# Kernel optimization log

Measured on AMD Instinct MI355X. Metric: run time of the kernel, lower is better.

The kernel has to match this reference:

```python
import jax, jax.numpy as jnp
import numpy as np

AXIAL_WEIGHT = 1.0
N_NODES = 1_000_000
N_ELEM = 2_000_000


def setup_inputs() -> dict:
    key = jax.random.key(0)
    ks = jax.random.split(key, 12)
    N, E = N_NODES, N_ELEM
    pred_raw = jax.random.normal(ks[0], (N, 3), jnp.float32)
    u_c = jax.random.uniform(ks[1], (1,), jnp.float32) + 0.5
    theta_c = jax.random.uniform(ks[2], (1,), jnp.float32) + 0.5
    connectivity = jax.random.randint(ks[3], (E, 2), 0, N, jnp.int32)
    # lengths / section properties bounded away from zero (1/L^3 appears)
    elem_lengths = jax.random.uniform(ks[4], (E,), jnp.float32) + 0.5
    prop_E = jax.random.uniform(ks[5], (E,), jnp.float32) + 1.0
    prop_A = jax.random.uniform(ks[6], (E,), jnp.float32) + 0.5
    prop_I22 = jax.random.uniform(ks[7], (E,), jnp.float32) + 0.5
    ang = jax.random.uniform(ks[8], (E,), jnp.float32) * (2.0 * np.pi)
    # columns: [cos, 0, sin] -- forward reads cols 0 and 2
    elem_directions = jnp.stack([jnp.cos(ang), jnp.zeros_like(ang), jnp.sin(ang)], axis=1)
    F_ext = jax.random.normal(ks[9], (N, 3), jnp.float32)
    bc_disp = (jax.random.uniform(ks[10], (N, 1)) < 0.05).astype(jnp.float32)
    bc_rot = (jax.random.uniform(ks[11], (N, 1)) < 0.05).astype(jnp.float32)
    return {
        "pred_raw": pred_raw, "u_c": u_c, "theta_c": theta_c,
        "elem_lengths": elem_lengths, "prop_E": prop_E, "prop_A": prop_A,
        "prop_I22": prop_I22, "elem_directions": elem_directions,
        "F_ext": F_ext, "bc_disp": bc_disp, "bc_rot": bc_rot,
        "connectivity": connectivity,
    }


def reference(pred_raw, u_c, theta_c, elem_lengths, prop_E, prop_A, prop_I22,
              elem_directions, F_ext, bc_disp, bc_rot, connectivity):
    n_nodes = pred_raw.shape[0]
    # physical displacements: [ux*u_c, uz*u_c, th*theta_c]
    scale = jnp.concatenate([u_c, u_c, theta_c])  # [3]
    u_phys = pred_raw * scale[None, :]

    nA = connectivity[:, 0]
    nB = connectivity[:, 1]
    c = elem_directions[:, 0]
    s = elem_directions[:, 2]
    L = elem_lengths
    EA = prop_E * prop_A
    EI = prop_E * prop_I22

    uA = u_phys[nA]  # [E,3] gather
    uB = u_phys[nB]
    u_A = c * uA[:, 0] + s * uA[:, 1]
    w_A = -s * uA[:, 0] + c * uA[:, 1]
    th_A = -uA[:, 2]
    u_B = c * uB[:, 0] + s * uB[:, 1]
    w_B = -s * uB[:, 0] + c * uB[:, 1]
    th_B = -uB[:, 2]

    ea_l = EA / L * AXIAL_WEIGHT
    ei_l = EI / L
    ei_l2 = EI / L**2
    ei_l3 = EI / L**3

    # analytic K_loc @ d_local (K_loc is the standard 6x6 beam stiffness)
    dw = w_A - w_B
    f0 = ea_l * (u_A - u_B)
    f1 = 12.0 * ei_l3 * dw + 6.0 * ei_l2 * (th_A + th_B)
    f2 = 6.0 * ei_l2 * dw + 4.0 * ei_l * th_A + 2.0 * ei_l * th_B
    f3 = -f0
    f4 = -f1
    f5 = 6.0 * ei_l2 * dw + 2.0 * ei_l * th_A + 4.0 * ei_l * th_B

    fA = jnp.stack([c * f0 - s * f1, s * f0 + c * f1, -f2], axis=1)  # [E,3]
    fB = jnp.stack([c * f3 - s * f4, s * f3 + c * f4, -f5], axis=1)

    F_int = jax.ops.segment_sum(
        jnp.concatenate([fA, fB], axis=0),
        jnp.concatenate([nA, nB], axis=0),
        num_segments=n_nodes)  # [N,3] scatter-add

    R = F_int - F_ext
    free_mask = jnp.concatenate([1.0 - bc_disp, 1.0 - bc_disp, 1.0 - bc_rot], axis=1)
    R_free = R * free_mask
    F_free = F_ext * free_mask
    F_norm_sq = jnp.maximum(jnp.sum(F_free**2), 1e-30)
    loss = jnp.sum(R_free**2) / F_norm_sq  # single graph -> n_graphs = 1
    return loss
```

## Files before the change

kernel.cpp:

```cpp
#include <hip/hip_runtime.h>
#include <hip/hip_fp16.h>


#define SPAN   1024
#define NBMAX  1024
#define OFFN   (NBMAX + 1)
#define FTH    1024
#define FBE    4096
#define REGR   8192
#define ATH    512

struct F3 { float x, y, z; };

__device__ __forceinline__ uint2 packrec(float fx, float fy, float fz, int local) {
    unsigned short hx = __half_as_ushort(__float2half(fx));
    unsigned short hy = __half_as_ushort(__float2half(fy));
    unsigned short hz = __half_as_ushort(__float2half(fz));
    return make_uint2(((unsigned)hy << 16) | hx, ((unsigned)local << 16) | hz);
}

__device__ __forceinline__ int block_incl_scan(int v, int* wsum, int lane, int wv) {
    #pragma unroll
    for (int off = 1; off < 64; off <<= 1) {
        int t = __shfl_up(v, off, 64);
        if (lane >= off) v += t;
    }
    if (lane == 63) wsum[wv] = v;
    __syncthreads();
    if (wv == 0) {
        int w = (lane < 16) ? wsum[lane] : 0;
        #pragma unroll
        for (int off = 1; off < 16; off <<= 1) {
            int t = __shfl_up(w, off, 64);
            if (lane >= off) w += t;
        }
        if (lane < 16) wsum[lane] = w;
    }
    __syncthreads();
    return v + ((wv > 0) ? wsum[wv - 1] : 0);
}

__global__ void __launch_bounds__(1024)
fill_kernel(const int2* __restrict__ conn,
            const F3*  __restrict__ pred,
            const float* __restrict__ u_c,
            const float* __restrict__ theta_c,
            const float* __restrict__ len,
            const float* __restrict__ pE,
            const float* __restrict__ pA,
            const float* __restrict__ pI,
            const float* __restrict__ dir,
            uint2* __restrict__ regions,
            unsigned short* __restrict__ offsTab,
            double* __restrict__ accSlots,
            int cs, int ce, int NB) {
    __shared__ uint2          slab[FBE];
    __shared__ unsigned short sbk [FBE];
    __shared__ int hist0[NBMAX];
    __shared__ int hist1[NBMAX];
    __shared__ int boff [NBMAX];
    __shared__ int sc   [NBMAX];
    __shared__ int wsum [16];

    int tid = threadIdx.x, lane = tid & 63, wv = tid >> 6;

    if (blockIdx.x == 0 && tid < 512) accSlots[tid] = 0.0;

    hist0[tid] = 0;
    hist1[tid] = 0;
    __syncthreads();

    float uc = u_c[0];
    float tc = theta_c[0];
    int bs = cs + blockIdx.x * FBE;
    int be = bs + FBE; if (be > ce) be = ce;

    unsigned sv[8];
    uint2    rc[8];

    #pragma unroll
    for (int j = 0; j < 4; ++j) {
        int e = bs + j * FTH + tid;
        unsigned sa = 0xFFFFFFFFu, sb = 0xFFFFFFFFu;
        if (e < be) {
            int2 cn = conn[e];
            int na = cn.x, nb = cn.y;

            F3 pa_ = pred[na];
            F3 pb_ = pred[nb];

            float c  = dir[3 * e + 0];
            float s  = dir[3 * e + 2];
            float L  = len[e];
            float Ee = pE[e];
            float EA = Ee * pA[e];
            float EI = Ee * pI[e];

            float a0 = pa_.x * uc;
            float a1 = pa_.y * uc;
            float a2 = pa_.z * tc;
            float b0 = pb_.x * uc;
            float b1 = pb_.y * uc;
            float b2 = pb_.z * tc;

            float u_A  =  c * a0 + s * a1;
            float w_A  = -s * a0 + c * a1;
            float th_A = -a2;
            float u_B  =  c * b0 + s * b1;
            float w_B  = -s * b0 + c * b1;
            float th_B = -b2;

            float invL  = 1.0f / L;
            float ea_l  = EA * invL;
            float ei_l  = EI * invL;
            float ei_l2 = ei_l  * invL;
            float ei_l3 = ei_l2 * invL;

            float dw = w_A - w_B;
            float f0 = ea_l * (u_A - u_B);
            float f1 = 12.0f * ei_l3 * dw + 6.0f * ei_l2 * (th_A + th_B);
            float f2 = 6.0f * ei_l2 * dw + 4.0f * ei_l * th_A + 2.0f * ei_l * th_B;
            float f5 = 6.0f * ei_l2 * dw + 2.0f * ei_l * th_A + 4.0f * ei_l * th_B;

            float fA0 = c * f0 - s * f1;
            float fA1 = s * f0 + c * f1;

            int* h = (j < 2) ? hist0 : hist1;

            int bkA = na >> 10;
            int rA  = atomicAdd(&h[bkA], 1);
            sa = ((unsigned)rA << 10) | (unsigned)bkA;
            rc[2 * j + 0] = packrec(fA0, fA1, -f2, na & 1023);

            int bkB = nb >> 10;
            int rB  = atomicAdd(&h[bkB], 1);
            sb = ((unsigned)rB << 10) | (unsigned)bkB;
            rc[2 * j + 1] = packrec(-fA0, -fA1, -f5, nb & 1023);
        }
        sv[2 * j + 0] = sa;
        sv[2 * j + 1] = sb;
    }
    __syncthreads();

    int h0 = hist0[tid], h1 = hist1[tid];
    int tot = h0 + h1;
    int iF = block_incl_scan(tot, wsum, lane, wv);
    boff[tid] = iF - tot;
    sc[tid]   = iF;
    __syncthreads();

    unsigned short* offs = offsTab + (size_t)blockIdx.x * OFFN;
    if (tid < NB) offs[tid] = (unsigned short)boff[tid];
    if (tid == 0) offs[NB]  = (unsigned short)sc[NB - 1];

    uint2* regbase = regions + (size_t)blockIdx.x * REGR;

    int i0 = block_incl_scan(h0, wsum, lane, wv);
    sc[tid] = i0;
    __syncthreads();
    #pragma unroll
    for (int r = 0; r < 4; ++r) {
        unsigned s2 = sv[r];
        if (s2 != 0xFFFFFFFFu) {
            int bk = (int)(s2 & 1023u);
            int rk = (int)(s2 >> 10);
            int slot = sc[bk] - hist0[bk] + rk;
            slab[slot] = rc[r];
            sbk[slot]  = (unsigned short)bk;
        }
    }
    __syncthreads();
    int tot0 = sc[NBMAX - 1];
    for (int i = tid; i < tot0; i += FTH) {
        int bk = sbk[i];
        regbase[boff[bk] + (i - (sc[bk] - hist0[bk]))] = slab[i];
    }
    __syncthreads();

    int i1 = block_incl_scan(h1, wsum, lane, wv);
    sc[tid] = i1;
    __syncthreads();
    #pragma unroll
    for (int r = 4; r < 8; ++r) {
        unsigned s2 = sv[r];
        if (s2 != 0xFFFFFFFFu) {
            int bk = (int)(s2 & 1023u);
            int rk = (int)(s2 >> 10);
            int slot = sc[bk] - hist1[bk] + rk;
            slab[slot] = rc[r];
            sbk[slot]  = (unsigned short)bk;
        }
    }
    __syncthreads();
    int tot1 = sc[NBMAX - 1];
    for (int i = tid; i < tot1; i += FTH) {
        int bk = sbk[i];
        regbase[boff[bk] + hist0[bk] + (i - (sc[bk] - hist1[bk]))] = slab[i];
    }
}

__global__ void __launch_bounds__(512)
accum_kernel(const uint2* __restrict__ regions,
             const unsigned short* __restrict__ offsTab,
             const float* __restrict__ Fext,
             const float* __restrict__ bcd,
             const float* __restrict__ bcr,
             double* __restrict__ accSlots,
             float* __restrict__ fint32,
             __half* __restrict__ fint16,
             int N, int NB, int NT, int isFirst, int isLast, int mode) {
    __shared__ float tile[SPAN * 3];
    __shared__ double sn[8], sd[8];

    int tid = threadIdx.x, lane = tid & 63, wv = tid >> 6;
    int b = blockIdx.x;
    int nodeLo = b * SPAN;
    int gBase = nodeLo * 3;
    int gMax  = 3 * N;

    if (isFirst) {
        for (int i = tid; i < SPAN * 3; i += ATH) tile[i] = 0.0f;
    } else if (mode == 1) {
        for (int i = tid; i < SPAN * 3; i += ATH) {
            int g = gBase + i;
            tile[i] = (g < gMax) ? fint32[g] : 0.0f;
        }
    } else {
        for (int i = tid; i < SPAN * 3; i += ATH) {
            int g = gBase + i;
            tile[i] = (g < gMax) ? __half2float(fint16[g]) : 0.0f;
        }
    }
    __syncthreads();

    if (tid < NT) {
        const unsigned short* o = offsTab + (size_t)tid * OFFN + b;
        int s0 = o[0];
        int s1 = o[1];
        const uint2* reg = regions + (size_t)tid * REGR;
        for (int i = s0; i < s1; ++i) {
            uint2 rec = reg[i];
            float fx = __half2float(__ushort_as_half((unsigned short)(rec.x & 0xFFFFu)));
            float fy = __half2float(__ushort_as_half((unsigned short)(rec.x >> 16)));
            float fz = __half2float(__ushort_as_half((unsigned short)(rec.y & 0xFFFFu)));
            int local = (int)(rec.y >> 16);
            atomicAdd(&tile[local * 3 + 0], fx);
            atomicAdd(&tile[local * 3 + 1], fy);
            atomicAdd(&tile[local * 3 + 2], fz);
        }
    }
    __syncthreads();

    if (!isLast) {
        if (mode == 1) {
            for (int i = tid; i < SPAN * 3; i += ATH) {
                int g = gBase + i;
                if (g < gMax) fint32[g] = tile[i];
            }
        } else {
            for (int i = tid; i < SPAN * 3; i += ATH) {
                int g = gBase + i;
                if (g < gMax) fint16[g] = __float2half(tile[i]);
            }
        }
        return;
    }

    int spanCnt = N - nodeLo;
    if (spanCnt > SPAN) spanCnt = SPAN;

    double num = 0.0, den = 0.0;
    for (int l = tid; l < spanCnt; l += ATH) {
        int n = nodeLo + l;
        float md = 1.0f - bcd[n];
        float mr = 1.0f - bcr[n];
        float e0 = Fext[3 * n + 0];
        float e1 = Fext[3 * n + 1];
        float e2 = Fext[3 * n + 2];
        float r0 = (tile[l * 3 + 0] - e0) * md;
        float r1 = (tile[l * 3 + 1] - e1) * md;
        float r2 = (tile[l * 3 + 2] - e2) * mr;
        float g0 = e0 * md;
        float g1 = e1 * md;
        float g2 = e2 * mr;
        num += (double)r0 * r0 + (double)r1 * r1 + (double)r2 * r2;
        den += (double)g0 * g0 + (double)g1 * g1 + (double)g2 * g2;
    }
    #pragma unroll
    for (int off = 32; off > 0; off >>= 1) {
        num += __shfl_down(num, off, 64);
        den += __shfl_down(den, off, 64);
    }
    if (lane == 0) { sn[wv] = num; sd[wv] = den; }
    __syncthreads();
    if (tid == 0) {
        double tn = 0.0, td = 0.0;
        #pragma unroll
        for (int w = 0; w < 8; ++w) { tn += sn[w]; td += sd[w]; }
        double* slot = accSlots + (size_t)(b & 63) * 8;
        atomicAdd(&slot[0], tn);
        atomicAdd(&slot[1], td);
    }
}

__global__ void final_kernel(const double* __restrict__ accSlots,
                             float* __restrict__ out) {
    int t = threadIdx.x;
    double n = accSlots[t * 8 + 0];
    double d = accSlots[t * 8 + 1];
    #pragma unroll
    for (int off = 32; off > 0; off >>= 1) {
        n += __shfl_down(n, off, 64);
        d += __shfl_down(d, off, 64);
    }
    if (t == 0) {
        if (d < 1e-30) d = 1e-30;
        out[0] = (float)(n / d);
    }
}

static inline size_t align256(size_t x) { return (x + 255) & ~(size_t)255; }

extern "C" void kernel_launch(void* const* d_in, const int* in_sizes, int n_in,
                              void* d_out, int out_size, void* d_ws, size_t ws_size,
                              hipStream_t stream) {
    const F3*    pred    = (const F3*)d_in[0];
    const float* u_c     = (const float*)d_in[1];
    const float* theta_c = (const float*)d_in[2];
    const float* len     = (const float*)d_in[3];
    const float* pE      = (const float*)d_in[4];
    const float* pA      = (const float*)d_in[5];
    const float* pI      = (const float*)d_in[6];
    const float* dir     = (const float*)d_in[7];
    const float* Fext    = (const float*)d_in[8];
    const float* bcd     = (const float*)d_in[9];
    const float* bcr     = (const float*)d_in[10];
    const int2*  conn    = (const int2*)d_in[11];

    int N = in_sizes[0] / 3;
    int E = in_sizes[3];
    int NB = (N + SPAN - 1) / SPAN;

    const int cfgK[7] = {1, 2, 2, 4, 4, 8, 16};
    const int cfgM[7] = {0, 1, 2, 1, 2, 2, 2};
    int K = 16, mode = 2;
    size_t oOff = 4096, oF = 0, oR = 0;
    for (int t = 0; t < 7; ++t) {
        int Kc = cfgK[t], Mc = cfgM[t];
        int ce = (E + Kc - 1) / Kc;
        int NTc = (ce + FBE - 1) / FBE;
        size_t offB = (size_t)NTc * OFFN * 2;
        size_t oFt  = align256(oOff + offB);
        size_t fb   = (Kc > 1) ? (size_t)3 * N * (Mc == 1 ? 4 : 2) : 0;
        size_t oRt  = align256(oFt + fb);
        size_t need = oRt + (size_t)NTc * REGR * 8;
        if (need <= ws_size || t == 6) {
            K = Kc; mode = Mc; oF = oFt; oR = oRt;
            if (need <= ws_size) break;
        }
    }

    int chunkElems = (E + K - 1) / K;

    double*         accSlots = (double*)d_ws;
    unsigned short* offsTab  = (unsigned short*)((char*)d_ws + oOff);
    float*          fint32   = (float*)((char*)d_ws + oF);
    __half*         fint16   = (__half*)((char*)d_ws + oF);
    uint2*          regions  = (uint2*)((char*)d_ws + oR);

    for (int c = 0; c < K; ++c) {
        int cs = c * chunkElems;
        if (cs >= E) break;
        int ce = cs + chunkElems;
        if (ce > E) ce = E;
        int NT = (ce - cs + FBE - 1) / FBE;

        fill_kernel<<<NT, FTH, 0, stream>>>(
            conn, pred, u_c, theta_c, len, pE, pA, pI, dir,
            regions, offsTab, accSlots, cs, ce, NB);

        int isFirst = (c == 0);
        int isLast  = (ce == E);
        accum_kernel<<<NB, ATH, 0, stream>>>(
            regions, offsTab, Fext, bcd, bcr, accSlots,
            fint32, fint16, N, NB, NT, isFirst, isLast, mode);
    }

    final_kernel<<<1, 64, 0, stream>>>(accSlots, (float*)d_out);
}
```

Before: 271.6 us.

## Replace per-block bucket regions with global counting-sort arena and coalesced accumulation

Adds count and scan passes that build a global per-bucket histogram, so the fill kernel reserves contiguous arena ranges through atomic cursors instead of writing per-block regions with offset tables. The accumulate kernel then reads each node span's records contiguously with all threads, rather than one thread walking each fill block's sub-range. Streaming inputs are read with nontemporal loads. This costs an extra read of connectivity plus zero, count and scan launches per chunk, and the order of records within a bucket is no longer deterministic.

```diff
diff --git a/kernel.cpp b/kernel.cpp
--- a/kernel.cpp
+++ b/kernel.cpp
@@ -4,11 +4,11 @@
 
 #define SPAN   1024
 #define NBMAX  1024
-#define OFFN   (NBMAX + 1)
+#define CURP   16
 #define FTH    1024
 #define FBE    4096
-#define REGR   8192
 #define ATH    512
+#define CB     256
 
 struct F3 { float x, y, z; };
 
@@ -41,7 +41,44 @@
 }
 
 __global__ void __launch_bounds__(1024)
-fill_kernel(const int2* __restrict__ conn,
+zero_kernel(int* __restrict__ p, int n) {
+    int i = blockIdx.x * 1024 + threadIdx.x;
+    if (i < n) p[i] = 0;
+}
+
+__global__ void __launch_bounds__(1024)
+count_kernel(const long long* __restrict__ conn, int* __restrict__ cnt,
+             int cs, int ce) {
+    __shared__ int h[NBMAX];
+    int tid = threadIdx.x;
+    h[tid] = 0;
+    __syncthreads();
+    int stride = gridDim.x * 1024;
+    for (int e = cs + blockIdx.x * 1024 + tid; e < ce; e += stride) {
+        long long v = __builtin_nontemporal_load(conn + e);
+        int na = (int)(unsigned)((unsigned long long)v & 0xFFFFFFFFull);
+        int nb = (int)(unsigned)((unsigned long long)v >> 32);
+        atomicAdd(&h[na >> 10], 1);
+        atomicAdd(&h[nb >> 10], 1);
+    }
+    __syncthreads();
+    int c = h[tid];
+    if (c) atomicAdd(&cnt[tid * CURP], c);
+}
+
+__global__ void __launch_bounds__(1024)
+scan_kernel(int* __restrict__ cnt, int* __restrict__ base) {
+    __shared__ int wsum[16];
+    int tid = threadIdx.x, lane = tid & 63, wv = tid >> 6;
+    int c = cnt[tid * CURP];
+    int incl = block_incl_scan(c, wsum, lane, wv);
+    base[tid + 1] = incl;
+    if (tid == 0) base[0] = 0;
+    cnt[tid * CURP] = incl - c;
+}
+
+__global__ void __launch_bounds__(1024)
+fill_kernel(const long long* __restrict__ conn,
             const F3*  __restrict__ pred,
             const float* __restrict__ u_c,
             const float* __restrict__ theta_c,
@@ -50,21 +87,18 @@
             const float* __restrict__ pA,
             const float* __restrict__ pI,
             const float* __restrict__ dir,
-            uint2* __restrict__ regions,
-            unsigned short* __restrict__ offsTab,
-            double* __restrict__ accSlots,
-            int cs, int ce, int NB) {
+            uint2* __restrict__ arena,
+            int* __restrict__ cursor,
+            int cs, int ce) {
     __shared__ uint2          slab[FBE];
     __shared__ unsigned short sbk [FBE];
     __shared__ int hist0[NBMAX];
     __shared__ int hist1[NBMAX];
-    __shared__ int boff [NBMAX];
     __shared__ int sc   [NBMAX];
+    __shared__ int astart[NBMAX];
     __shared__ int wsum [16];
 
     int tid = threadIdx.x, lane = tid & 63, wv = tid >> 6;
-
-    if (blockIdx.x == 0 && tid < 512) accSlots[tid] = 0.0;
 
     hist0[tid] = 0;
     hist1[tid] = 0;
@@ -83,18 +117,19 @@
         int e = bs + j * FTH + tid;
         unsigned sa = 0xFFFFFFFFu, sb = 0xFFFFFFFFu;
         if (e < be) {
-            int2 cn = conn[e];
-            int na = cn.x, nb = cn.y;
+            long long cv = __builtin_nontemporal_load(conn + e);
+            int na = (int)(unsigned)((unsigned long long)cv & 0xFFFFFFFFull);
+            int nb = (int)(unsigned)((unsigned long long)cv >> 32);
 
             F3 pa_ = pred[na];
             F3 pb_ = pred[nb];
 
-            float c  = dir[3 * e + 0];
-            float s  = dir[3 * e + 2];
-            float L  = len[e];
-            float Ee = pE[e];
-            float EA = Ee * pA[e];
-            float EI = Ee * pI[e];
+            float c  = __builtin_nontemporal_load(&dir[3 * e + 0]);
+            float s  = __builtin_nontemporal_load(&dir[3 * e + 2]);
+            float L  = __builtin_nontemporal_load(&len[e]);
+            float Ee = __builtin_nontemporal_load(&pE[e]);
+            float EA = Ee * __builtin_nontemporal_load(&pA[e]);
+            float EI = Ee * __builtin_nontemporal_load(&pI[e]);
 
             float a0 = pa_.x * uc;
             float a1 = pa_.y * uc;
@@ -144,16 +179,7 @@
 
     int h0 = hist0[tid], h1 = hist1[tid];
     int tot = h0 + h1;
-    int iF = block_incl_scan(tot, wsum, lane, wv);
-    boff[tid] = iF - tot;
-    sc[tid]   = iF;
-    __syncthreads();
-
-    unsigned short* offs = offsTab + (size_t)blockIdx.x * OFFN;
-    if (tid < NB) offs[tid] = (unsigned short)boff[tid];
-    if (tid == 0) offs[NB]  = (unsigned short)sc[NB - 1];
-
-    uint2* regbase = regions + (size_t)blockIdx.x * REGR;
+    if (tot) astart[tid] = atomicAdd(&cursor[tid * CURP], tot);
 
     int i0 = block_incl_scan(h0, wsum, lane, wv);
     sc[tid] = i0;
@@ -173,7 +199,7 @@
     int tot0 = sc[NBMAX - 1];
     for (int i = tid; i < tot0; i += FTH) {
         int bk = sbk[i];
-        regbase[boff[bk] + (i - (sc[bk] - hist0[bk]))] = slab[i];
+        arena[astart[bk] + (i - (sc[bk] - hist0[bk]))] = slab[i];
     }
     __syncthreads();
 
@@ -195,20 +221,20 @@
     int tot1 = sc[NBMAX - 1];
     for (int i = tid; i < tot1; i += FTH) {
         int bk = sbk[i];
-        regbase[boff[bk] + hist0[bk] + (i - (sc[bk] - hist1[bk]))] = slab[i];
+        arena[astart[bk] + hist0[bk] + (i - (sc[bk] - hist1[bk]))] = slab[i];
     }
 }
 
 __global__ void __launch_bounds__(512)
-accum_kernel(const uint2* __restrict__ regions,
-             const unsigned short* __restrict__ offsTab,
+accum_kernel(const unsigned long long* __restrict__ arena,
+             const int* __restrict__ base,
              const float* __restrict__ Fext,
              const float* __restrict__ bcd,
              const float* __restrict__ bcr,
              double* __restrict__ accSlots,
              float* __restrict__ fint32,
              __half* __restrict__ fint16,
-             int N, int NB, int NT, int isFirst, int isLast, int mode) {
+             int N, int isFirst, int isLast, int mode) {
     __shared__ float tile[SPAN * 3];
     __shared__ double sn[8], sd[8];
 
@@ -233,21 +259,19 @@
     }
     __syncthreads();
 
-    if (tid < NT) {
-        const unsigned short* o = offsTab + (size_t)tid * OFFN + b;
-        int s0 = o[0];
-        int s1 = o[1];
-        const uint2* reg = regions + (size_t)tid * REGR;
-        for (int i = s0; i < s1; ++i) {
-            uint2 rec = reg[i];
-            float fx = __half2float(__ushort_as_half((unsigned short)(rec.x & 0xFFFFu)));
-            float fy = __half2float(__ushort_as_half((unsigned short)(rec.x >> 16)));
-            float fz = __half2float(__ushort_as_half((unsigned short)(rec.y & 0xFFFFu)));
-            int local = (int)(rec.y >> 16);
-            atomicAdd(&tile[local * 3 + 0], fx);
-            atomicAdd(&tile[local * 3 + 1], fy);
-            atomicAdd(&tile[local * 3 + 2], fz);
-        }
+    int s0 = base[b];
+    int s1 = base[b + 1];
+    for (int i = s0 + tid; i < s1; i += ATH) {
+        unsigned long long rv = __builtin_nontemporal_load(arena + i);
+        unsigned lo = (unsigned)(rv & 0xFFFFFFFFull);
+        unsigned hi = (unsigned)(rv >> 32);
+        float fx = __half2float(__ushort_as_half((unsigned short)(lo & 0xFFFFu)));
+        float fy = __half2float(__ushort_as_half((unsigned short)(lo >> 16)));
+        float fz = __half2float(__ushort_as_half((unsigned short)(hi & 0xFFFFu)));
+        int local = (int)(hi >> 16);
+        atomicAdd(&tile[local * 3 + 0], fx);
+        atomicAdd(&tile[local * 3 + 1], fy);
+        atomicAdd(&tile[local * 3 + 2], fz);
     }
     __syncthreads();
 
@@ -272,11 +296,11 @@
     double num = 0.0, den = 0.0;
     for (int l = tid; l < spanCnt; l += ATH) {
         int n = nodeLo + l;
-        float md = 1.0f - bcd[n];
-        float mr = 1.0f - bcr[n];
-        float e0 = Fext[3 * n + 0];
-        float e1 = Fext[3 * n + 1];
-        float e2 = Fext[3 * n + 2];
+        float md = 1.0f - __builtin_nontemporal_load(&bcd[n]);
+        float mr = 1.0f - __builtin_nontemporal_load(&bcr[n]);
+        float e0 = __builtin_nontemporal_load(&Fext[3 * n + 0]);
+        float e1 = __builtin_nontemporal_load(&Fext[3 * n + 1]);
+        float e2 = __builtin_nontemporal_load(&Fext[3 * n + 2]);
         float r0 = (tile[l * 3 + 0] - e0) * md;
         float r1 = (tile[l * 3 + 1] - e1) * md;
         float r2 = (tile[l * 3 + 2] - e2) * mr;
@@ -335,38 +359,44 @@
     const float* Fext    = (const float*)d_in[8];
     const float* bcd     = (const float*)d_in[9];
     const float* bcr     = (const float*)d_in[10];
-    const int2*  conn    = (const int2*)d_in[11];
+    const long long* conn = (const long long*)d_in[11];
 
     int N = in_sizes[0] / 3;
     int E = in_sizes[3];
     int NB = (N + SPAN - 1) / SPAN;
 
-    const int cfgK[7] = {1, 2, 2, 4, 4, 8, 16};
-    const int cfgM[7] = {0, 1, 2, 1, 2, 2, 2};
-    int K = 16, mode = 2;
-    size_t oOff = 4096, oF = 0, oR = 0;
-    for (int t = 0; t < 7; ++t) {
+    size_t oCnt  = 4096;
+    size_t oBase = oCnt + (size_t)NBMAX * CURP * 4;
+    size_t oFint0 = align256(oBase + 4 * (NBMAX + 1));
+
+    const int cfgK[6] = {1, 2, 2, 4, 4, 8};
+    const int cfgM[6] = {0, 1, 2, 1, 2, 2};
+    int K = 8, mode = 2;
+    size_t oF = oFint0, oA = oFint0;
+    for (int t = 0; t < 6; ++t) {
         int Kc = cfgK[t], Mc = cfgM[t];
-        int ce = (E + Kc - 1) / Kc;
-        int NTc = (ce + FBE - 1) / FBE;
-        size_t offB = (size_t)NTc * OFFN * 2;
-        size_t oFt  = align256(oOff + offB);
-        size_t fb   = (Kc > 1) ? (size_t)3 * N * (Mc == 1 ? 4 : 2) : 0;
-        size_t oRt  = align256(oFt + fb);
-        size_t need = oRt + (size_t)NTc * REGR * 8;
-        if (need <= ws_size || t == 6) {
-            K = Kc; mode = Mc; oF = oFt; oR = oRt;
+        size_t chunkE = (size_t)(E + Kc - 1) / Kc;
+        size_t fsz = (Kc > 1) ? (size_t)3 * N * (Mc == 1 ? 4 : 2) : 0;
+        size_t oAt = align256(oFint0 + fsz);
+        size_t need = oAt + 2 * chunkE * 8;
+        if (need <= ws_size || t == 5) {
+            K = Kc; mode = Mc; oF = oFint0; oA = oAt;
             if (need <= ws_size) break;
         }
     }
 
     int chunkElems = (E + K - 1) / K;
 
-    double*         accSlots = (double*)d_ws;
-    unsigned short* offsTab  = (unsigned short*)((char*)d_ws + oOff);
-    float*          fint32   = (float*)((char*)d_ws + oF);
-    __half*         fint16   = (__half*)((char*)d_ws + oF);
-    uint2*          regions  = (uint2*)((char*)d_ws + oR);
+    double*             accSlots = (double*)d_ws;
+    int*                cnt      = (int*)((char*)d_ws + oCnt);
+    int*                base     = (int*)((char*)d_ws + oBase);
+    float*              fint32   = (float*)((char*)d_ws + oF);
+    __half*             fint16   = (__half*)((char*)d_ws + oF);
+    uint2*              arena    = (uint2*)((char*)d_ws + oA);
+    unsigned long long* arenaLL  = (unsigned long long*)arena;
+
+    int zeroWordsAll = (int)(oBase / 4);
+    int zeroWordsCnt = (int)((oBase - oCnt) / 4);
 
     for (int c = 0; c < K; ++c) {
         int cs = c * chunkElems;
@@ -375,15 +405,24 @@
         if (ce > E) ce = E;
         int NT = (ce - cs + FBE - 1) / FBE;
 
+        if (c == 0) {
+            zero_kernel<<<(zeroWordsAll + 1023) / 1024, 1024, 0, stream>>>(
+                (int*)d_ws, zeroWordsAll);
+        } else {
+            zero_kernel<<<(zeroWordsCnt + 1023) / 1024, 1024, 0, stream>>>(
+                cnt, zeroWordsCnt);
+        }
+        count_kernel<<<CB, 1024, 0, stream>>>(conn, cnt, cs, ce);
+        scan_kernel<<<1, 1024, 0, stream>>>(cnt, base);
         fill_kernel<<<NT, FTH, 0, stream>>>(
             conn, pred, u_c, theta_c, len, pE, pA, pI, dir,
-            regions, offsTab, accSlots, cs, ce, NB);
+            arena, cnt, cs, ce);
 
         int isFirst = (c == 0);
         int isLast  = (ce == E);
         accum_kernel<<<NB, ATH, 0, stream>>>(
-            regions, offsTab, Fext, bcd, bcr, accSlots,
-            fint32, fint16, N, NB, NT, isFirst, isLast, mode);
+            arenaLL, base, Fext, bcd, bcr, accSlots,
+            fint32, fint16, N, isFirst, isLast, mode);
     }
 
     final_kernel<<<1, 64, 0, stream>>>(accSlots, (float*)d_out);
```

After: 296.5 us. 9.2% more time.
